# Performance work log

Hardware: AMD Instinct MI355X
Metric: run time of the kernel (lower is better)

## Reference

```python
import jax, jax.numpy as jnp
import numpy as np

N, C, F = 16384, 2048, 512


def setup_inputs() -> dict:
    key = jax.random.key(0)
    kx, km = jax.random.split(key)
    x = jax.random.normal(kx, (N, F), dtype=jnp.float32)
    means = jax.random.normal(km, (C, F), dtype=jnp.float32)
    return {"x": x, "means": means}


def reference(x, means):
    # Negative Euclidean distance scores: -sqrt(sum_f (x[n,f] - means[c,f])^2)
    # intermediate the naive expand/pow/sum formulation materializes).
    x_sq = jnp.sum(x * x, axis=-1, keepdims=True)          # [N, 1]
    m_sq = jnp.sum(means * means, axis=-1)                 # [C]
    cross = jnp.einsum('nf,cf->nc', x, means)              # [N, C]
    d2 = jnp.maximum(x_sq + m_sq[None, :] - 2.0 * cross, 0.0)
    return -jnp.sqrt(d2)
```

## Files before the change

kernel.cpp:

```cpp
#include <hip/hip_runtime.h>
#include <hip/hip_bf16.h>

constexpr int N_ROWS = 16384;
constexpr int C_CLS  = 2048;
constexpr int F_DIM  = 512;

typedef __bf16 bf16x8 __attribute__((ext_vector_type(8)));
typedef float  f32x16 __attribute__((ext_vector_type(16)));

__global__ __launch_bounds__(256) void prep_rows(
    const float* __restrict__ src,
    __hip_bfloat162* __restrict__ dst,
    float* __restrict__ sq)
{
    const int row = blockIdx.x;
    const int tid = threadIdx.x;
    const float2 v = ((const float2*)(src + (size_t)row * F_DIM))[tid];

    __hip_bfloat162 p;
    p.x = __float2bfloat16(v.x);
    p.y = __float2bfloat16(v.y);
    dst[(size_t)row * (F_DIM / 2) + tid] = p;

    float ss = v.x * v.x + v.y * v.y;
    #pragma unroll
    for (int off = 32; off > 0; off >>= 1) ss += __shfl_down(ss, off);

    __shared__ float red[4];
    if ((tid & 63) == 0) red[tid >> 6] = ss;
    __syncthreads();
    if (tid == 0) sq[row] = red[0] + red[1] + red[2] + red[3];
}

__device__ __forceinline__ void async_copy16(const __hip_bfloat16* g,
                                             __hip_bfloat16* l)
{
    __builtin_amdgcn_global_load_lds(
        (const __attribute__((address_space(1))) unsigned int*)g,
        (__attribute__((address_space(3))) unsigned int*)l,
        16, 0, 0);
}

__global__ __launch_bounds__(256) void ncm_gemm(
    const __hip_bfloat16* __restrict__ xb,
    const __hip_bfloat16* __restrict__ mb,
    const float* __restrict__ xsq,
    const float* __restrict__ msq,
    float* __restrict__ out)
{
    constexpr int BM = 128, BN = 128, BK = 64;

    __shared__ alignas(16) __hip_bfloat16 sA[BM * BK];
    __shared__ alignas(16) __hip_bfloat16 sB[BN * BK];

    const int tid  = threadIdx.x;
    const int wave = tid >> 6;
    const int lane = tid & 63;
    const int wm   = wave >> 1;
    const int wn   = wave & 1;

    const int row0 = blockIdx.y * BM;
    const int col0 = blockIdx.x * BN;

    const int srow   = lane >> 3;
    const int schunk = (lane & 7) ^ srow;
    const int scol   = schunk * 8;

    const __hip_bfloat16* gA =
        xb + (size_t)(row0 + wave * 32 + srow) * F_DIM + scol;
    const __hip_bfloat16* gB =
        mb + (size_t)(col0 + wave * 32 + srow) * F_DIM + scol;

    f32x16 acc[2][2] = {};

    const int lrow  = lane & 31;
    const int khalf = lane >> 5;

    for (int kt = 0; kt < F_DIM / BK; ++kt) {
        const int k0 = kt * BK;
        #pragma unroll
        for (int i = 0; i < 4; ++i) {
            async_copy16(gA + (size_t)i * 8 * F_DIM + k0,
                         &sA[(wave * 32 + i * 8) * BK]);
            async_copy16(gB + (size_t)i * 8 * F_DIM + k0,
                         &sB[(wave * 32 + i * 8) * BK]);
        }
        __syncthreads();

        #pragma unroll
        for (int s = 0; s < 4; ++s) {
            const int pos = ((2 * s + khalf) ^ (lane & 7)) * 8;
            bf16x8 af[2], bfr[2];
            #pragma unroll
            for (int mt = 0; mt < 2; ++mt)
                af[mt] = *(const bf16x8*)
                    &sA[(wm * 64 + mt * 32 + lrow) * BK + pos];
            #pragma unroll
            for (int nt = 0; nt < 2; ++nt)
                bfr[nt] = *(const bf16x8*)
                    &sB[(wn * 64 + nt * 32 + lrow) * BK + pos];
            #pragma unroll
            for (int mt = 0; mt < 2; ++mt)
                #pragma unroll
                for (int nt = 0; nt < 2; ++nt)
                    acc[mt][nt] = __builtin_amdgcn_mfma_f32_32x32x16_bf16(
                        af[mt], bfr[nt], acc[mt][nt], 0, 0, 0);
        }
        __syncthreads();
    }

    #pragma unroll
    for (int mt = 0; mt < 2; ++mt) {
        const int rbase = row0 + wm * 64 + mt * 32 + 4 * khalf;
        float xs[16];
        #pragma unroll
        for (int r = 0; r < 16; ++r)
            xs[r] = xsq[rbase + (r & 3) + 8 * (r >> 2)];
        #pragma unroll
        for (int nt = 0; nt < 2; ++nt) {
            const int col = col0 + wn * 64 + nt * 32 + lrow;
            const float ms = msq[col];
            #pragma unroll
            for (int r = 0; r < 16; ++r) {
                const int row = rbase + (r & 3) + 8 * (r >> 2);
                const float d2 =
                    fmaxf(xs[r] + ms - 2.0f * acc[mt][nt][r], 0.0f);
                out[(size_t)row * C_CLS + col] = -sqrtf(d2);
            }
        }
    }
}

extern "C" void kernel_launch(void* const* d_in, const int* in_sizes, int n_in,
                              void* d_out, int out_size, void* d_ws,
                              size_t ws_size, hipStream_t stream)
{
    const float* x     = (const float*)d_in[0];
    const float* means = (const float*)d_in[1];
    float* out = (float*)d_out;

    char* ws = (char*)d_ws;
    __hip_bfloat16* xb = (__hip_bfloat16*)ws;
    __hip_bfloat16* mb = (__hip_bfloat16*)(ws + (size_t)N_ROWS * F_DIM * 2);
    float* xsq = (float*)(ws + (size_t)(N_ROWS + C_CLS) * F_DIM * 2);
    float* msq = xsq + N_ROWS;

    prep_rows<<<N_ROWS, 256, 0, stream>>>(x, (__hip_bfloat162*)xb, xsq);
    prep_rows<<<C_CLS, 256, 0, stream>>>(means, (__hip_bfloat162*)mb, msq);

    dim3 grid(C_CLS / 128, N_ROWS / 128);
    ncm_gemm<<<grid, 256, 0, stream>>>(xb, mb, xsq, msq, out);
}
```

Measured before the change: 209.2 us.

## Double-buffer A tile in LDS, load B fragments directly to registers, merge prep launches

The GEMM now double-buffers the x tile in shared memory, prefetching the next K-slice asynchronously while computing on the current one. This removes one barrier per iteration and overlaps loads with MFMA work. The means operand is no longer staged in LDS; each wave reads its B fragments straight from global memory into registers, relying on L2/cache reuse rather than shared-memory reuse. The two prep launches are merged into one grid to save a launch. The trade-off is that B is fetched redundantly by the two wave rows and global-load latency is exposed on the critical path.

```diff
diff --git a/kernel.cpp b/kernel.cpp
--- a/kernel.cpp
+++ b/kernel.cpp
@@ -9,11 +9,20 @@
 typedef float  f32x16 __attribute__((ext_vector_type(16)));
 
 __global__ __launch_bounds__(256) void prep_rows(
-    const float* __restrict__ src,
-    __hip_bfloat162* __restrict__ dst,
-    float* __restrict__ sq)
+    const float* __restrict__ x,
+    const float* __restrict__ means,
+    __hip_bfloat162* __restrict__ xb,
+    __hip_bfloat162* __restrict__ mb,
+    float* __restrict__ xsq,
+    float* __restrict__ msq)
 {
-    const int row = blockIdx.x;
+    int row = blockIdx.x;
+    const float* src;
+    __hip_bfloat162* dst;
+    float* sq;
+    if (row < N_ROWS) { src = x; dst = xb; sq = xsq; }
+    else { row -= N_ROWS; src = means; dst = mb; sq = msq; }
+
     const int tid = threadIdx.x;
     const float2 v = ((const float2*)(src + (size_t)row * F_DIM))[tid];
 
@@ -48,10 +57,9 @@
     const float* __restrict__ msq,
     float* __restrict__ out)
 {
-    constexpr int BM = 128, BN = 128, BK = 64;
+    constexpr int BM = 128, BK = 64, NKT = F_DIM / BK;
 
-    __shared__ alignas(16) __hip_bfloat16 sA[BM * BK];
-    __shared__ alignas(16) __hip_bfloat16 sB[BN * BK];
+    __shared__ alignas(16) __hip_bfloat16 sA[2][BM * BK];
 
     const int tid  = threadIdx.x;
     const int wave = tid >> 6;
@@ -60,53 +68,60 @@
     const int wn   = wave & 1;
 
     const int row0 = blockIdx.y * BM;
-    const int col0 = blockIdx.x * BN;
+    const int col0 = blockIdx.x * 128;
 
     const int srow   = lane >> 3;
     const int schunk = (lane & 7) ^ srow;
-    const int scol   = schunk * 8;
+    const __hip_bfloat16* gA =
+        xb + (size_t)(row0 + wave * 32 + srow) * F_DIM + schunk * 8;
 
-    const __hip_bfloat16* gA =
-        xb + (size_t)(row0 + wave * 32 + srow) * F_DIM + scol;
+    const int lrow  = lane & 31;
+    const int khalf = lane >> 5;
     const __hip_bfloat16* gB =
-        mb + (size_t)(col0 + wave * 32 + srow) * F_DIM + scol;
+        mb + (size_t)(col0 + wn * 64 + lrow) * F_DIM + khalf * 8;
 
     f32x16 acc[2][2] = {};
 
-    const int lrow  = lane & 31;
-    const int khalf = lane >> 5;
+    #pragma unroll
+    for (int i = 0; i < 4; ++i)
+        async_copy16(gA + (size_t)i * 8 * F_DIM,
+                     &sA[0][(wave * 32 + i * 8) * BK]);
 
-    for (int kt = 0; kt < F_DIM / BK; ++kt) {
-        const int k0 = kt * BK;
+    for (int kt = 0; kt < NKT; ++kt) {
+        const int p = kt & 1;
+        __syncthreads();
+
+        if (kt + 1 < NKT) {
+            const int k0n = (kt + 1) * BK;
+            #pragma unroll
+            for (int i = 0; i < 4; ++i)
+                async_copy16(gA + (size_t)i * 8 * F_DIM + k0n,
+                             &sA[1 - p][(wave * 32 + i * 8) * BK]);
+        }
+
+        bf16x8 bfr[4][2];
         #pragma unroll
-        for (int i = 0; i < 4; ++i) {
-            async_copy16(gA + (size_t)i * 8 * F_DIM + k0,
-                         &sA[(wave * 32 + i * 8) * BK]);
-            async_copy16(gB + (size_t)i * 8 * F_DIM + k0,
-                         &sB[(wave * 32 + i * 8) * BK]);
-        }
-        __syncthreads();
+        for (int s = 0; s < 4; ++s)
+            #pragma unroll
+            for (int nt = 0; nt < 2; ++nt)
+                bfr[s][nt] = *(const bf16x8*)
+                    (gB + (size_t)nt * 32 * F_DIM + kt * BK + s * 16);
 
         #pragma unroll
         for (int s = 0; s < 4; ++s) {
             const int pos = ((2 * s + khalf) ^ (lane & 7)) * 8;
-            bf16x8 af[2], bfr[2];
+            bf16x8 af[2];
             #pragma unroll
             for (int mt = 0; mt < 2; ++mt)
                 af[mt] = *(const bf16x8*)
-                    &sA[(wm * 64 + mt * 32 + lrow) * BK + pos];
-            #pragma unroll
-            for (int nt = 0; nt < 2; ++nt)
-                bfr[nt] = *(const bf16x8*)
-                    &sB[(wn * 64 + nt * 32 + lrow) * BK + pos];
+                    &sA[p][(wm * 64 + mt * 32 + lrow) * BK + pos];
             #pragma unroll
             for (int mt = 0; mt < 2; ++mt)
                 #pragma unroll
                 for (int nt = 0; nt < 2; ++nt)
                     acc[mt][nt] = __builtin_amdgcn_mfma_f32_32x32x16_bf16(
-                        af[mt], bfr[nt], acc[mt][nt], 0, 0, 0);
+                        af[mt], bfr[s][nt], acc[mt][nt], 0, 0, 0);
         }
-        __syncthreads();
     }
 
     #pragma unroll
@@ -145,8 +160,8 @@
     float* xsq = (float*)(ws + (size_t)(N_ROWS + C_CLS) * F_DIM * 2);
     float* msq = xsq + N_ROWS;
 
-    prep_rows<<<N_ROWS, 256, 0, stream>>>(x, (__hip_bfloat162*)xb, xsq);
-    prep_rows<<<C_CLS, 256, 0, stream>>>(means, (__hip_bfloat162*)mb, msq);
+    prep_rows<<<N_ROWS + C_CLS, 256, 0, stream>>>(
+        x, means, (__hip_bfloat162*)xb, (__hip_bfloat162*)mb, xsq, msq);
 
     dim3 grid(C_CLS / 128, N_ROWS / 128);
     ncm_gemm<<<grid, 256, 0, stream>>>(xb, mb, xsq, msq, out);
```

Result: slower. 227.8 us (+8.9%).
